# Kernel optimization log

Measured on AMD Instinct MI355X. Metric: run time of the kernel, lower is better.

Reference implementation:

```python
import jax, jax.numpy as jnp
import numpy as np

NUM_EXPERTS = 64
TOP_K = 2
MAX_SEQ_LENGTH = 4096
CAPACITY_FACTOR = 1.0
EXPERT_CAPACITY = int(CAPACITY_FACTOR * (MAX_SEQ_LENGTH * TOP_K) / NUM_EXPERTS)  # 128


def setup_inputs() -> dict:
    key = jax.random.key(0)
    k1, k2 = jax.random.split(key)
    hidden_states = jax.random.normal(k1, (8, 4096, 4096), dtype=jnp.float32)
    router_weight = jax.random.normal(k2, (NUM_EXPERTS, 4096), dtype=jnp.float32) * 0.02
    return {"hidden_states": hidden_states, "router_weight": router_weight}


def reference(hidden_states, router_weight):
    B, S, H = hidden_states.shape
    E, K, C = NUM_EXPERTS, TOP_K, EXPERT_CAPACITY

    # router projection + softmax
    router_logits = jnp.einsum('bsh,eh->bse', hidden_states, router_weight)
    router_probs = jax.nn.softmax(router_logits, axis=-1)

    # top-k experts per token, renormalized weights
    expert_weights, expert_indices = jax.lax.top_k(router_probs, K)  # [B,S,K]
    expert_weights = expert_weights / jnp.sum(expert_weights, axis=-1, keepdims=True)

    # Capacity-limited dispatch. The torch loops process slot k=0 for all tokens
    # (in seq order), then k=1, with a shared per-(batch,expert) counter that
    # saturates at capacity. Equivalent: order tokens k-major-then-seq, take an
    # exclusive cumsum of one-hot assignments, and keep entries with prior
    # attempt count < capacity.
    oh = jax.nn.one_hot(expert_indices, E, dtype=jnp.int32)        # [B,S,K,E]
    oh_ord = oh.transpose(0, 2, 1, 3).reshape(B, K * S, E)         # k-major ordering
    pos = jnp.cumsum(oh_ord, axis=1) - oh_ord                      # exclusive cumsum [B,KS,E]
    keep = ((pos < C) & (oh_ord == 1)).astype(hidden_states.dtype) # [B,KS,E]
    keep = keep.reshape(B, K, S, E)

    dispatch_tensor = jnp.sum(keep, axis=1)                                      # [B,S,E]
    combine_tensor = jnp.einsum('bkse,bsk->bse', keep, expert_weights)           # [B,S,E]

    aux_loss = jnp.mean(jnp.sum(router_probs * router_probs, axis=-1)) * E
    z_loss = jnp.mean(jax.scipy.special.logsumexp(router_logits, axis=-1) ** 2)
    return dispatch_tensor, combine_tensor, router_probs, aux_loss, z_loss
```

## Files before the change

### kernel.cpp

```cpp
#include <hip/hip_runtime.h>
#include <math.h>

#define NE 64
#define TPB 64
#define KC 64
#define HDIM 4096
#define SEQ 4096
#define NTOK 32768
#define CAP 128
#define LS 68
#define AMB_TH 2.0e-3f

__global__ __launch_bounds__(256) void k_router(
    const float* __restrict__ hs, const float* __restrict__ rw,
    float* __restrict__ dispatch, float* __restrict__ combine,
    float* __restrict__ probs_out,
    int* __restrict__ idx_buf, float* __restrict__ wgt_buf,
    float* __restrict__ partials,
    int* __restrict__ fix_cnt, int* __restrict__ fix_list)
{
    __shared__ float shh[KC * LS];
    __shared__ float sww[KC * LS];
    __shared__ float red1[4], red2[4];

    const int tid = threadIdx.x;
    const int tokBase = blockIdx.x * TPB;

    const int eg = tid & 15;
    const int tg = tid >> 4;

    float acc[4][4];
#pragma unroll
    for (int i = 0; i < 4; ++i)
#pragma unroll
        for (int j = 0; j < 4; ++j) acc[i][j] = 0.f;

    const int r_ld  = tid & 63;
    const int k_off = (tid >> 6) * 16;
    const float* hrow = hs + (size_t)(tokBase + r_ld) * HDIM + k_off;
    const float* wrow = rw + (size_t)r_ld * HDIM + k_off;

    float4 hreg[4], wreg[4];
#pragma unroll
    for (int i = 0; i < 4; ++i) hreg[i] = *(const float4*)(hrow + i * 4);
#pragma unroll
    for (int i = 0; i < 4; ++i) wreg[i] = *(const float4*)(wrow + i * 4);

    const int nChunks = HDIM / KC;
    for (int c = 0; c < nChunks; ++c) {
        __syncthreads();
#pragma unroll
        for (int i = 0; i < 4; ++i) {
            const int kk = k_off + i * 4;
            shh[(kk + 0) * LS + r_ld] = hreg[i].x;
            shh[(kk + 1) * LS + r_ld] = hreg[i].y;
            shh[(kk + 2) * LS + r_ld] = hreg[i].z;
            shh[(kk + 3) * LS + r_ld] = hreg[i].w;
            sww[(kk + 0) * LS + r_ld] = wreg[i].x;
            sww[(kk + 1) * LS + r_ld] = wreg[i].y;
            sww[(kk + 2) * LS + r_ld] = wreg[i].z;
            sww[(kk + 3) * LS + r_ld] = wreg[i].w;
        }
        __syncthreads();
        if (c + 1 < nChunks) {
            const float* hp = hrow + (size_t)(c + 1) * KC;
            const float* wp = wrow + (size_t)(c + 1) * KC;
#pragma unroll
            for (int i = 0; i < 4; ++i) hreg[i] = *(const float4*)(hp + i * 4);
#pragma unroll
            for (int i = 0; i < 4; ++i) wreg[i] = *(const float4*)(wp + i * 4);
        }
#pragma unroll 8
        for (int k = 0; k < KC; ++k) {
            const float4 h = *(const float4*)&shh[k * LS + 4 * tg];
            const float4 w = *(const float4*)&sww[k * LS + 4 * eg];
            const float hv[4] = {h.x, h.y, h.z, h.w};
            const float wv[4] = {w.x, w.y, w.z, w.w};
#pragma unroll
            for (int i = 0; i < 4; ++i)
#pragma unroll
                for (int j = 0; j < 4; ++j)
                    acc[i][j] = fmaf(hv[i], wv[j], acc[i][j]);
        }
    }

    __syncthreads();
#pragma unroll
    for (int i = 0; i < 4; ++i)
#pragma unroll
        for (int j = 0; j < 4; ++j)
            shh[(4 * tg + i) * LS + 4 * eg + j] = acc[i][j];
    __syncthreads();

    {
        const float4 z4 = make_float4(0.f, 0.f, 0.f, 0.f);
        float4* dp = (float4*)(dispatch + (size_t)tokBase * NE);
        float4* cp = (float4*)(combine + (size_t)tokBase * NE);
#pragma unroll
        for (int m = 0; m < 4; ++m) {
            dp[m * 256 + tid] = z4;
            cp[m * 256 + tid] = z4;
        }
    }

    float p2 = 0.f, zl = 0.f;
    if (tid < TPB) {
        const float* rowl = &shh[tid * LS];

        float b0 = -3.4e38f, b1 = -3.4e38f, b2 = -3.4e38f;
        int i0 = 0, i1 = 0;
#pragma unroll
        for (int e = 0; e < NE; ++e) {
            const float l = rowl[e];
            if (l > b0)      { b2 = b1; b1 = b0; i1 = i0; b0 = l; i0 = e; }
            else if (l > b1) { b2 = b1; b1 = l; i1 = e; }
            else if (l > b2) { b2 = l; }
        }

        float fp[NE];
        float sum = 0.f;
#pragma unroll
        for (int e = 0; e < NE; ++e) {
            const float s = expf(rowl[e] - b0);
            sum += s;
            fp[e] = s;
        }
        const float inv = 1.f / sum;
        float p2l = 0.f;
#pragma unroll
        for (int e = 0; e < NE; ++e) {
            const float p = fp[e] * inv;
            fp[e] = p;
            p2l += p * p;
        }
        float4* gp = (float4*)(probs_out + (size_t)(tokBase + tid) * NE);
#pragma unroll
        for (int q = 0; q < 16; ++q) gp[q] = *(float4*)&fp[4 * q];

        p2 = p2l;
        const float lse = b0 + logf(sum);
        zl = lse * lse;

        const float w0 = 1.f / (1.f + expf(b1 - b0));
        const float w1 = 1.f / (1.f + expf(b0 - b1));
        idx_buf[(size_t)(tokBase + tid) * 2 + 0] = i0;
        idx_buf[(size_t)(tokBase + tid) * 2 + 1] = i1;
        wgt_buf[(size_t)(tokBase + tid) * 2 + 0] = w0;
        wgt_buf[(size_t)(tokBase + tid) * 2 + 1] = w1;

        if ((b0 - b1 < AMB_TH) || (b1 - b2 < AMB_TH)) {
            const int p = atomicAdd(fix_cnt, 1);
            fix_list[p] = tokBase + tid;
        }
    }

#pragma unroll
    for (int off = 32; off; off >>= 1) {
        p2 += __shfl_down(p2, off);
        zl += __shfl_down(zl, off);
    }
    const int lane = tid & 63, wid = tid >> 6;
    if (lane == 0) { red1[wid] = p2; red2[wid] = zl; }
    __syncthreads();
    if (tid == 0) {
        partials[blockIdx.x * 2 + 0] = red1[0] + red1[1] + red1[2] + red1[3];
        partials[blockIdx.x * 2 + 1] = red2[0] + red2[1] + red2[2] + red2[3];
    }
}

__global__ __launch_bounds__(256) void k_fixup(
    const float* __restrict__ hs, const float* __restrict__ rw,
    const int* __restrict__ fix_cnt, const int* __restrict__ fix_list,
    int* __restrict__ idx_buf, float* __restrict__ wgt_buf)
{
    __shared__ double part[NE][5];
    __shared__ double lg[NE];
    const int tid = threadIdx.x;
    const int e  = tid & 63;
    const int kq = tid >> 6;
    const int n = fix_cnt[0];

    for (int fi = blockIdx.x; fi < n; fi += gridDim.x) {
        const int t = fix_list[fi];
        const float4* hp = (const float4*)(hs + (size_t)t * HDIM + kq * 1024);
        const float4* wp = (const float4*)(rw + (size_t)e * HDIM + kq * 1024);
        double a = 0.0;
#pragma unroll 4
        for (int i = 0; i < 256; ++i) {
            const float4 h = hp[i];
            const float4 w = wp[i];
            a = fma((double)h.x, (double)w.x, a);
            a = fma((double)h.y, (double)w.y, a);
            a = fma((double)h.z, (double)w.z, a);
            a = fma((double)h.w, (double)w.w, a);
        }
        part[e][kq] = a;
        __syncthreads();
        if (tid < NE)
            lg[tid] = part[tid][0] + part[tid][1] + part[tid][2] + part[tid][3];
        __syncthreads();
        if (tid == 0) {
            double b0 = -1.0e300, b1 = -1.0e300;
            int i0 = 0, i1 = 0;
            for (int x = 0; x < NE; ++x) {
                const double l = lg[x];
                if (l > b0)      { b1 = b0; i1 = i0; b0 = l; i0 = x; }
                else if (l > b1) { b1 = l; i1 = x; }
            }
            const double w0 = 1.0 / (1.0 + exp(b1 - b0));
            const double w1 = 1.0 / (1.0 + exp(b0 - b1));
            idx_buf[(size_t)t * 2 + 0] = i0;
            idx_buf[(size_t)t * 2 + 1] = i1;
            wgt_buf[(size_t)t * 2 + 0] = (float)w0;
            wgt_buf[(size_t)t * 2 + 1] = (float)w1;
        }
        __syncthreads();
    }
}

__global__ __launch_bounds__(256) void k_dispatch(
    const int* __restrict__ idx_buf, const float* __restrict__ wgt_buf,
    float* __restrict__ dispatch, float* __restrict__ combine)
{
    const int e = blockIdx.x & 63;
    const int b = blockIdx.x >> 6;
    __shared__ int wc[4];
    const int tid = threadIdx.x;
    const int lane = tid & 63, wid = tid >> 6;
    const int base = b * SEQ;

    int running = 0;
    for (int chunk = 0; chunk < 32; ++chunk) {
        int j = chunk * 256 + tid;
        int k = j >> 12;
        int s = j & (SEQ - 1);
        int my = idx_buf[(size_t)(base + s) * 2 + k];
        bool m = (my == e);
        unsigned long long bal = __ballot(m);
        int prefix = __popcll(bal & ((1ull << lane) - 1ull));
        if (lane == 0) wc[wid] = __popcll(bal);
        __syncthreads();
        int woff = 0, tot = 0;
#pragma unroll
        for (int w = 0; w < 4; ++w) {
            int c = wc[w];
            tot += c;
            if (w < wid) woff += c;
        }
        if (m) {
            int pos = running + woff + prefix;
            if (pos < CAP) {
                size_t o = (size_t)(base + s) * NE + e;
                dispatch[o] = 1.0f;
                combine[o] = wgt_buf[(size_t)(base + s) * 2 + k];
            }
        }
        running += tot;
        __syncthreads();
    }
}

__global__ __launch_bounds__(256) void k_final(
    const float* __restrict__ partials, float* __restrict__ out)
{
    __shared__ float r1[4], r2[4];
    const int tid = threadIdx.x;
    float a = partials[tid * 2 + 0] + partials[(tid + 256) * 2 + 0];
    float b = partials[tid * 2 + 1] + partials[(tid + 256) * 2 + 1];
#pragma unroll
    for (int off = 32; off; off >>= 1) {
        a += __shfl_down(a, off);
        b += __shfl_down(b, off);
    }
    const int lane = tid & 63, wid = tid >> 6;
    if (lane == 0) { r1[wid] = a; r2[wid] = b; }
    __syncthreads();
    if (tid == 0) {
        float at = r1[0] + r1[1] + r1[2] + r1[3];
        float bt = r2[0] + r2[1] + r2[2] + r2[3];
        out[0] = at / (float)NTOK * (float)NE;
        out[1] = bt / (float)NTOK;
    }
}

extern "C" void kernel_launch(void* const* d_in, const int* in_sizes, int n_in,
                              void* d_out, int out_size, void* d_ws, size_t ws_size,
                              hipStream_t stream)
{
    const float* hs = (const float*)d_in[0];
    const float* rw = (const float*)d_in[1];
    float* out = (float*)d_out;
    float* dispatch = out;
    float* combine  = out + 2097152;
    float* probs    = out + 2 * 2097152;
    float* scalars  = out + 3 * 2097152;

    int*   idx_buf  = (int*)d_ws;
    float* wgt_buf  = (float*)((char*)d_ws + 65536 * 4);
    float* partials = (float*)((char*)d_ws + 65536 * 8);
    int*   fix_cnt  = (int*)((char*)d_ws + 65536 * 8 + 4096);
    int*   fix_list = (int*)((char*)d_ws + 65536 * 8 + 8192);

    hipMemsetAsync(fix_cnt, 0, sizeof(int), stream);
    hipLaunchKernelGGL(k_router, dim3(NTOK / TPB), dim3(256), 0, stream,
                       hs, rw, dispatch, combine, probs, idx_buf, wgt_buf,
                       partials, fix_cnt, fix_list);
    hipLaunchKernelGGL(k_fixup, dim3(256), dim3(256), 0, stream,
                       hs, rw, fix_cnt, fix_list, idx_buf, wgt_buf);
    hipLaunchKernelGGL(k_dispatch, dim3(8 * NE), dim3(256), 0, stream,
                       idx_buf, wgt_buf, dispatch, combine);
    hipLaunchKernelGGL(k_final, dim3(1), dim3(256), 0, stream,
                       partials, scalars);
}
```

Before: 951.5 us.

## Use split-bf16 MFMA for router GEMM, fuse fixup, wave-per-expert dispatch

Replaces the FP32 FMA router GEMM with bf16 MFMA 16x16x32 instructions using a hi/lo split (three products) to keep near-FP32 accuracy. The router weights are pre-split by a new prep kernel, and operands are double-buffered through LDS with register prefetch. The separate fixup kernel for near-tie tokens is folded into the router block using a block-local flag list. The dispatch kernel now gives each expert one wave and exits early once capacity is reached. The split-bf16 products add conversion work and some rounding differences, and the in-block fixup serializes fp64 recomputation inside the affected blocks.

Result: slower. 1.074 ms (+12.8%).

```diff
diff --git a/kernel.cpp b/kernel.cpp
--- a/kernel.cpp
+++ b/kernel.cpp
@@ -3,99 +3,184 @@
 
 #define NE 64
 #define TPB 64
-#define KC 64
 #define HDIM 4096
 #define SEQ 4096
 #define NTOK 32768
 #define CAP 128
-#define LS 68
+#define LSW 88
+#define LSF 68
 #define AMB_TH 2.0e-3f
 
+typedef __attribute__((ext_vector_type(8))) short bf16x8;
+typedef __attribute__((ext_vector_type(4))) float f32x4;
+typedef __attribute__((ext_vector_type(4))) unsigned short us4;
+
+__device__ __forceinline__ unsigned short bf16_rtne(float f) {
+    unsigned u = __float_as_uint(f);
+    return (unsigned short)((u + 0x7FFFu + ((u >> 16) & 1u)) >> 16);
+}
+__device__ __forceinline__ void split2(float f, unsigned short& hi, unsigned short& lo) {
+    unsigned u = __float_as_uint(f);
+    unsigned r = (u + 0x7FFFu + ((u >> 16) & 1u)) & 0xFFFF0000u;
+    hi = (unsigned short)(r >> 16);
+    lo = bf16_rtne(f - __uint_as_float(r));
+}
+
+__global__ __launch_bounds__(256) void k_prep(
+    const float* __restrict__ rw,
+    unsigned short* __restrict__ wh, unsigned short* __restrict__ wl)
+{
+    const size_t base = (size_t)blockIdx.x * HDIM + threadIdx.x * 16;
+#pragma unroll
+    for (int i = 0; i < 4; ++i) {
+        const f32x4 v = *(const f32x4*)(rw + base + i * 4);
+        us4 h4, l4;
+#pragma unroll
+        for (int j = 0; j < 4; ++j) {
+            unsigned short hh, ll;
+            split2(v[j], hh, ll);
+            h4[j] = hh;
+            l4[j] = ll;
+        }
+        *(us4*)(wh + base + i * 4) = h4;
+        *(us4*)(wl + base + i * 4) = l4;
+    }
+}
+
 __global__ __launch_bounds__(256) void k_router(
-    const float* __restrict__ hs, const float* __restrict__ rw,
+    const float* __restrict__ hs,
+    const unsigned short* __restrict__ wh, const unsigned short* __restrict__ wl,
+    const float* __restrict__ rw,
     float* __restrict__ dispatch, float* __restrict__ combine,
     float* __restrict__ probs_out,
     int* __restrict__ idx_buf, float* __restrict__ wgt_buf,
-    float* __restrict__ partials,
-    int* __restrict__ fix_cnt, int* __restrict__ fix_list)
-{
-    __shared__ float shh[KC * LS];
-    __shared__ float sww[KC * LS];
+    float* __restrict__ partials)
+{
+    __shared__ short sw[2][2][64 * LSW];
+    __shared__ double dpart[NE][4];
     __shared__ float red1[4], red2[4];
-
-    const int tid = threadIdx.x;
+    __shared__ int nflag, flist[64];
+
+    const int tid  = threadIdx.x;
+    const int wv   = tid >> 6;
+    const int lane = tid & 63;
+    const int lr   = lane & 15;
+    const int kg   = lane >> 4;
     const int tokBase = blockIdx.x * TPB;
 
-    const int eg = tid & 15;
-    const int tg = tid >> 4;
-
-    float acc[4][4];
-#pragma unroll
-    for (int i = 0; i < 4; ++i)
-#pragma unroll
-        for (int j = 0; j < 4; ++j) acc[i][j] = 0.f;
-
-    const int r_ld  = tid & 63;
-    const int k_off = (tid >> 6) * 16;
-    const float* hrow = hs + (size_t)(tokBase + r_ld) * HDIM + k_off;
-    const float* wrow = rw + (size_t)r_ld * HDIM + k_off;
-
-    float4 hreg[4], wreg[4];
-#pragma unroll
-    for (int i = 0; i < 4; ++i) hreg[i] = *(const float4*)(hrow + i * 4);
-#pragma unroll
-    for (int i = 0; i < 4; ++i) wreg[i] = *(const float4*)(wrow + i * 4);
-
-    const int nChunks = HDIM / KC;
-    for (int c = 0; c < nChunks; ++c) {
-        __syncthreads();
-#pragma unroll
-        for (int i = 0; i < 4; ++i) {
-            const int kk = k_off + i * 4;
-            shh[(kk + 0) * LS + r_ld] = hreg[i].x;
-            shh[(kk + 1) * LS + r_ld] = hreg[i].y;
-            shh[(kk + 2) * LS + r_ld] = hreg[i].z;
-            shh[(kk + 3) * LS + r_ld] = hreg[i].w;
-            sww[(kk + 0) * LS + r_ld] = wreg[i].x;
-            sww[(kk + 1) * LS + r_ld] = wreg[i].y;
-            sww[(kk + 2) * LS + r_ld] = wreg[i].z;
-            sww[(kk + 3) * LS + r_ld] = wreg[i].w;
-        }
-        __syncthreads();
-        if (c + 1 < nChunks) {
-            const float* hp = hrow + (size_t)(c + 1) * KC;
-            const float* wp = wrow + (size_t)(c + 1) * KC;
-#pragma unroll
-            for (int i = 0; i < 4; ++i) hreg[i] = *(const float4*)(hp + i * 4);
-#pragma unroll
-            for (int i = 0; i < 4; ++i) wreg[i] = *(const float4*)(wp + i * 4);
-        }
-#pragma unroll 8
-        for (int k = 0; k < KC; ++k) {
-            const float4 h = *(const float4*)&shh[k * LS + 4 * tg];
-            const float4 w = *(const float4*)&sww[k * LS + 4 * eg];
-            const float hv[4] = {h.x, h.y, h.z, h.w};
-            const float wv[4] = {w.x, w.y, w.z, w.w};
-#pragma unroll
-            for (int i = 0; i < 4; ++i)
-#pragma unroll
-                for (int j = 0; j < 4; ++j)
-                    acc[i][j] = fmaf(hv[i], wv[j], acc[i][j]);
-        }
-    }
-
-    __syncthreads();
-#pragma unroll
-    for (int i = 0; i < 4; ++i)
-#pragma unroll
-        for (int j = 0; j < 4; ++j)
-            shh[(4 * tg + i) * LS + 4 * eg + j] = acc[i][j];
+    if (tid == 0) nflag = 0;
+
+    f32x4 acc[4];
+#pragma unroll
+    for (int t = 0; t < 4; ++t) acc[t] = (f32x4){0.f, 0.f, 0.f, 0.f};
+
+    const float* hrow = hs + (size_t)(tokBase + wv * 16 + lr) * HDIM + kg * 8;
+
+    const int we = tid & 63;
+    const int wq = tid >> 6;
+    const int wp = wq >> 1;
+    const int wk = (wq & 1) * 32;
+    const unsigned short* wsrc = (wp ? wl : wh) + (size_t)we * HDIM + wk;
+    short* wdst0 = &sw[0][wp][we * LSW + wk];
+    short* wdst1 = &sw[1][wp][we * LSW + wk];
+
+    f32x4 hrA[4], hrB[4];
+    bf16x8 wrA[4], wrB[4];
+
+#pragma unroll
+    for (int i = 0; i < 4; ++i) wrA[i] = *(const bf16x8*)(wsrc + i * 8);
+#pragma unroll
+    for (int s = 0; s < 2; ++s)
+#pragma unroll
+        for (int h2 = 0; h2 < 2; ++h2)
+            hrA[s * 2 + h2] = *(const f32x4*)(hrow + s * 32 + h2 * 4);
+#pragma unroll
+    for (int i = 0; i < 4; ++i) *(bf16x8*)(wdst0 + i * 8) = wrA[i];
+#pragma unroll
+    for (int i = 0; i < 4; ++i) wrB[i] = *(const bf16x8*)(wsrc + 64 + i * 8);
+#pragma unroll
+    for (int s = 0; s < 2; ++s)
+#pragma unroll
+        for (int h2 = 0; h2 < 2; ++h2)
+            hrB[s * 2 + h2] = *(const f32x4*)(hrow + 64 + s * 32 + h2 * 4);
+    __syncthreads();
+
+#define CONVERT_A(HR, AH, AL)                                              \
+    {                                                                      \
+        _Pragma("unroll")                                                  \
+        for (int s = 0; s < 2; ++s) {                                      \
+            _Pragma("unroll")                                              \
+            for (int j = 0; j < 8; ++j) {                                  \
+                unsigned short hi_, lo_;                                   \
+                split2(HR[s * 2 + (j >> 2)][j & 3], hi_, lo_);             \
+                AH[s][j] = (short)hi_;                                     \
+                AL[s][j] = (short)lo_;                                     \
+            }                                                              \
+        }                                                                  \
+    }
+
+#define MFMA_PHASE(BUF, AH, AL)                                            \
+    {                                                                      \
+        _Pragma("unroll")                                                  \
+        for (int s = 0; s < 2; ++s) {                                      \
+            _Pragma("unroll")                                              \
+            for (int t = 0; t < 4; ++t) {                                  \
+                const bf16x8 bh = *(const bf16x8*)&sw[BUF][0][(t * 16 + lr) * LSW + s * 32 + kg * 8]; \
+                const bf16x8 bl = *(const bf16x8*)&sw[BUF][1][(t * 16 + lr) * LSW + s * 32 + kg * 8]; \
+                acc[t] = __builtin_amdgcn_mfma_f32_16x16x32_bf16(AH[s], bh, acc[t], 0, 0, 0); \
+                acc[t] = __builtin_amdgcn_mfma_f32_16x16x32_bf16(AH[s], bl, acc[t], 0, 0, 0); \
+                acc[t] = __builtin_amdgcn_mfma_f32_16x16x32_bf16(AL[s], bh, acc[t], 0, 0, 0); \
+            }                                                              \
+        }                                                                  \
+    }
+
+    bf16x8 ahi[2], alo[2];
+    for (int c = 0; c < 64; c += 2) {
+        CONVERT_A(hrA, ahi, alo)
+#pragma unroll
+        for (int i = 0; i < 4; ++i) *(bf16x8*)(wdst1 + i * 8) = wrB[i];
+        {
+            const int cn = (c + 2 < 64) ? c + 2 : 63;
+#pragma unroll
+            for (int i = 0; i < 4; ++i) wrA[i] = *(const bf16x8*)(wsrc + cn * 64 + i * 8);
+#pragma unroll
+            for (int s = 0; s < 2; ++s)
+#pragma unroll
+                for (int h2 = 0; h2 < 2; ++h2)
+                    hrA[s * 2 + h2] = *(const f32x4*)(hrow + cn * 64 + s * 32 + h2 * 4);
+        }
+        MFMA_PHASE(0, ahi, alo)
+        __syncthreads();
+
+        CONVERT_A(hrB, ahi, alo)
+#pragma unroll
+        for (int i = 0; i < 4; ++i) *(bf16x8*)(wdst0 + i * 8) = wrA[i];
+        {
+            const int cn = (c + 3 < 64) ? c + 3 : 63;
+#pragma unroll
+            for (int i = 0; i < 4; ++i) wrB[i] = *(const bf16x8*)(wsrc + cn * 64 + i * 8);
+#pragma unroll
+            for (int s = 0; s < 2; ++s)
+#pragma unroll
+                for (int h2 = 0; h2 < 2; ++h2)
+                    hrB[s * 2 + h2] = *(const f32x4*)(hrow + cn * 64 + s * 32 + h2 * 4);
+        }
+        MFMA_PHASE(1, ahi, alo)
+        __syncthreads();
+    }
+
+    float* lgd = (float*)&sw[0][0][0];
+#pragma unroll
+    for (int t = 0; t < 4; ++t)
+#pragma unroll
+        for (int r = 0; r < 4; ++r)
+            lgd[(wv * 16 + kg * 4 + r) * LSF + t * 16 + lr] = acc[t][r];
     __syncthreads();
 
     {
-        const float4 z4 = make_float4(0.f, 0.f, 0.f, 0.f);
-        float4* dp = (float4*)(dispatch + (size_t)tokBase * NE);
-        float4* cp = (float4*)(combine + (size_t)tokBase * NE);
+        const f32x4 z4 = (f32x4){0.f, 0.f, 0.f, 0.f};
+        f32x4* dp = (f32x4*)(dispatch + (size_t)tokBase * NE);
+        f32x4* cp = (f32x4*)(combine + (size_t)tokBase * NE);
 #pragma unroll
         for (int m = 0; m < 4; ++m) {
             dp[m * 256 + tid] = z4;
@@ -105,7 +190,7 @@
 
     float p2 = 0.f, zl = 0.f;
     if (tid < TPB) {
-        const float* rowl = &shh[tid * LS];
+        const float* rowl = &lgd[tid * LSF];
 
         float b0 = -3.4e38f, b1 = -3.4e38f, b2 = -3.4e38f;
         int i0 = 0, i1 = 0;
@@ -133,9 +218,9 @@
             fp[e] = p;
             p2l += p * p;
         }
-        float4* gp = (float4*)(probs_out + (size_t)(tokBase + tid) * NE);
-#pragma unroll
-        for (int q = 0; q < 16; ++q) gp[q] = *(float4*)&fp[4 * q];
+        f32x4* gp = (f32x4*)(probs_out + (size_t)(tokBase + tid) * NE);
+#pragma unroll
+        for (int q = 0; q < 16; ++q) gp[q] = *(f32x4*)&fp[4 * q];
 
         p2 = p2l;
         const float lse = b0 + logf(sum);
@@ -149,8 +234,8 @@
         wgt_buf[(size_t)(tokBase + tid) * 2 + 1] = w1;
 
         if ((b0 - b1 < AMB_TH) || (b1 - b2 < AMB_TH)) {
-            const int p = atomicAdd(fix_cnt, 1);
-            fix_list[p] = tokBase + tid;
+            const int p = atomicAdd(&nflag, 1);
+            flist[p] = tid;
         }
     }
 
@@ -159,51 +244,39 @@
         p2 += __shfl_down(p2, off);
         zl += __shfl_down(zl, off);
     }
-    const int lane = tid & 63, wid = tid >> 6;
-    if (lane == 0) { red1[wid] = p2; red2[wid] = zl; }
+    if (lane == 0) { red1[wv] = p2; red2[wv] = zl; }
     __syncthreads();
     if (tid == 0) {
         partials[blockIdx.x * 2 + 0] = red1[0] + red1[1] + red1[2] + red1[3];
         partials[blockIdx.x * 2 + 1] = red2[0] + red2[1] + red2[2] + red2[3];
     }
-}
-
-__global__ __launch_bounds__(256) void k_fixup(
-    const float* __restrict__ hs, const float* __restrict__ rw,
-    const int* __restrict__ fix_cnt, const int* __restrict__ fix_list,
-    int* __restrict__ idx_buf, float* __restrict__ wgt_buf)
-{
-    __shared__ double part[NE][5];
-    __shared__ double lg[NE];
-    const int tid = threadIdx.x;
-    const int e  = tid & 63;
-    const int kq = tid >> 6;
-    const int n = fix_cnt[0];
-
-    for (int fi = blockIdx.x; fi < n; fi += gridDim.x) {
-        const int t = fix_list[fi];
-        const float4* hp = (const float4*)(hs + (size_t)t * HDIM + kq * 1024);
-        const float4* wp = (const float4*)(rw + (size_t)e * HDIM + kq * 1024);
+
+    __syncthreads();
+    const int nf = nflag;
+    for (int f = 0; f < nf; ++f) {
+        const int t = tokBase + flist[f];
+        const float* hp  = hs + (size_t)t * HDIM + wq * 1024;
+        const float* wp2 = rw + (size_t)we * HDIM + wq * 1024;
         double a = 0.0;
 #pragma unroll 4
         for (int i = 0; i < 256; ++i) {
-            const float4 h = hp[i];
-            const float4 w = wp[i];
-            a = fma((double)h.x, (double)w.x, a);
-            a = fma((double)h.y, (double)w.y, a);
-            a = fma((double)h.z, (double)w.z, a);
-            a = fma((double)h.w, (double)w.w, a);
-        }
-        part[e][kq] = a;
+            const f32x4 hv = *(const f32x4*)(hp + i * 4);
+            const f32x4 wv4 = *(const f32x4*)(wp2 + i * 4);
+            a = fma((double)hv[0], (double)wv4[0], a);
+            a = fma((double)hv[1], (double)wv4[1], a);
+            a = fma((double)hv[2], (double)wv4[2], a);
+            a = fma((double)hv[3], (double)wv4[3], a);
+        }
+        dpart[we][wq] = a;
         __syncthreads();
         if (tid < NE)
-            lg[tid] = part[tid][0] + part[tid][1] + part[tid][2] + part[tid][3];
+            dpart[tid][0] = dpart[tid][0] + dpart[tid][1] + dpart[tid][2] + dpart[tid][3];
         __syncthreads();
         if (tid == 0) {
             double b0 = -1.0e300, b1 = -1.0e300;
             int i0 = 0, i1 = 0;
             for (int x = 0; x < NE; ++x) {
-                const double l = lg[x];
+                const double l = dpart[x][0];
                 if (l > b0)      { b1 = b0; i1 = i0; b0 = l; i0 = x; }
                 else if (l > b1) { b1 = l; i1 = x; }
             }
@@ -222,41 +295,30 @@
     const int* __restrict__ idx_buf, const float* __restrict__ wgt_buf,
     float* __restrict__ dispatch, float* __restrict__ combine)
 {
-    const int e = blockIdx.x & 63;
-    const int b = blockIdx.x >> 6;
-    __shared__ int wc[4];
-    const int tid = threadIdx.x;
-    const int lane = tid & 63, wid = tid >> 6;
+    const int gw = (blockIdx.x << 2) | (threadIdx.x >> 6);
+    const int e = gw & 63;
+    const int b = gw >> 6;
+    const int lane = threadIdx.x & 63;
     const int base = b * SEQ;
 
     int running = 0;
-    for (int chunk = 0; chunk < 32; ++chunk) {
-        int j = chunk * 256 + tid;
-        int k = j >> 12;
-        int s = j & (SEQ - 1);
-        int my = idx_buf[(size_t)(base + s) * 2 + k];
-        bool m = (my == e);
-        unsigned long long bal = __ballot(m);
-        int prefix = __popcll(bal & ((1ull << lane) - 1ull));
-        if (lane == 0) wc[wid] = __popcll(bal);
-        __syncthreads();
-        int woff = 0, tot = 0;
-#pragma unroll
-        for (int w = 0; w < 4; ++w) {
-            int c = wc[w];
-            tot += c;
-            if (w < wid) woff += c;
-        }
+    for (int chunk = 0; chunk < 128; ++chunk) {
+        const int j = (chunk << 6) | lane;
+        const int k = j >> 12;
+        const int s = j & (SEQ - 1);
+        const int my = idx_buf[(size_t)(base + s) * 2 + k];
+        const bool m = (my == e);
+        const unsigned long long bal = __ballot(m);
         if (m) {
-            int pos = running + woff + prefix;
+            const int pos = running + __popcll(bal & ((1ull << lane) - 1ull));
             if (pos < CAP) {
-                size_t o = (size_t)(base + s) * NE + e;
+                const size_t o = (size_t)(base + s) * NE + e;
                 dispatch[o] = 1.0f;
                 combine[o] = wgt_buf[(size_t)(base + s) * 2 + k];
             }
         }
-        running += tot;
-        __syncthreads();
+        running += __popcll(bal);
+        if (running >= CAP) break;
     }
 }
 
@@ -296,18 +358,16 @@
     float* scalars  = out + 3 * 2097152;
 
     int*   idx_buf  = (int*)d_ws;
-    float* wgt_buf  = (float*)((char*)d_ws + 65536 * 4);
-    float* partials = (float*)((char*)d_ws + 65536 * 8);
-    int*   fix_cnt  = (int*)((char*)d_ws + 65536 * 8 + 4096);
-    int*   fix_list = (int*)((char*)d_ws + 65536 * 8 + 8192);
-
-    hipMemsetAsync(fix_cnt, 0, sizeof(int), stream);
+    float* wgt_buf  = (float*)((char*)d_ws + 262144);
+    float* partials = (float*)((char*)d_ws + 524288);
+    unsigned short* whbuf = (unsigned short*)((char*)d_ws + 786432);
+    unsigned short* wlbuf = (unsigned short*)((char*)d_ws + 1310720);
+
+    hipLaunchKernelGGL(k_prep, dim3(NE), dim3(256), 0, stream, rw, whbuf, wlbuf);
     hipLaunchKernelGGL(k_router, dim3(NTOK / TPB), dim3(256), 0, stream,
-                       hs, rw, dispatch, combine, probs, idx_buf, wgt_buf,
-                       partials, fix_cnt, fix_list);
-    hipLaunchKernelGGL(k_fixup, dim3(256), dim3(256), 0, stream,
-                       hs, rw, fix_cnt, fix_list, idx_buf, wgt_buf);
-    hipLaunchKernelGGL(k_dispatch, dim3(8 * NE), dim3(256), 0, stream,
+                       hs, whbuf, wlbuf, rw, dispatch, combine, probs,
+                       idx_buf, wgt_buf, partials);
+    hipLaunchKernelGGL(k_dispatch, dim3(128), dim3(256), 0, stream,
                        idx_buf, wgt_buf, dispatch, combine);
     hipLaunchKernelGGL(k_final, dim3(1), dim3(256), 0, stream,
                        partials, scalars);
```
